# Performance work log

Hardware: AMD Instinct MI355X
Metric: run time of the kernel (lower is better)

Reference implementation:

```python
import jax, jax.numpy as jnp
import numpy as np

EPS = 1e-4  # SPDRectifiedLinear eigenvalue threshold
POOL = 17   # adaptive pool output size


def setup_inputs() -> dict:
    key = jax.random.key(0)
    ks = jax.random.split(key, 6)
    B, Cin, H, W = 32, 2048, 34, 34
    Cr = 256
    feat_dim = Cr * (Cr + 1) // 2  # 32896
    x = jax.random.normal(ks[0], (B, Cin, H, W), dtype=jnp.float32)
    W_red = jax.random.normal(ks[1], (Cr, Cin), dtype=jnp.float32) * (1.0 / np.sqrt(Cin))
    W1 = jax.random.normal(ks[2], (256, feat_dim), dtype=jnp.float32) * (1.0 / np.sqrt(feat_dim))
    b1 = jax.random.normal(ks[3], (256,), dtype=jnp.float32) * 0.01
    W2 = jax.random.normal(ks[4], (3, 256), dtype=jnp.float32) * (1.0 / np.sqrt(256.0))
    b2 = jax.random.normal(ks[5], (3,), dtype=jnp.float32) * 0.01
    return {"x": x, "W_red": W_red, "W1": W1, "b1": b1, "W2": W2, "b2": b2}


def reference(x, W_red, W1, b1, W2, b2):
    B, Cin, H, W = x.shape
    # AdaptiveAvgPool2d((17,17)) with H=W=34 is exactly a uniform 2x2 avg pool
    f = x.reshape(B, Cin, POOL, H // POOL, POOL, W // POOL).mean(axis=(3, 5))  # [B,Cin,17,17]
    # 1x1 conv (no bias) == channel-mixing matmul
    f = jnp.einsum('bchw,dc->bdhw', f, W_red)  # [B,Cr,17,17]
    Cr = f.shape[1]
    f = f.reshape(B, Cr, -1).transpose(0, 2, 1)  # [B, N=289, Cr]
    N = f.shape[1]
    # batch covariance over spatial positions (unbiased)
    xc = f - f.mean(axis=1, keepdims=True)
    cov = jnp.einsum('bnc,bnd->bcd', xc, xc) / (N - 1)  # [B,Cr,Cr] SPD
    # SPD ReLU (eigenvalue clamp at EPS) followed by SPD logmap (matrix log)
    # share one eigendecomposition: same eigenvectors for both ops
    w, v = jnp.linalg.eigh(cov)
    w = jnp.log(jnp.clip(w, EPS))
    cov = jnp.einsum('bic,bc,bjc->bij', v, w, v)  # log-mapped symmetric matrix
    # SPD flatten: upper triangle, off-diagonal scaled by sqrt(2)
    iu, ju = jnp.triu_indices(Cr)
    scale = jnp.where(iu == ju, 1.0, jnp.sqrt(2.0)).astype(cov.dtype)
    flat = cov[:, iu, ju] * scale  # [B, Cr*(Cr+1)/2]
    # classifier MLP
    h = jax.nn.relu(flat @ W1.T + b1)
    return h @ W2.T + b2  # [B, num_classes]
```

## Files before the change

### kernel.cpp

```cpp
#include <hip/hip_runtime.h>
#include <math.h>


#define SWEEPS 7
#define NROUNDS (SWEEPS * 15)

#define P_OFF     0
#define A_OFF     0
#define V_OFF     8388608
#define U_OFF     16777216
#define LOGW_OFF  17825792
#define MEAN_OFF  79691776
#define F_OFF     83558400
#define FLAT_OFF  83558400
#define PART_OFF  93519872
#define H_OFF     94568448
#define WS_REQUIRED 94601216

__device__ __forceinline__ void pair16(int r, int t, int& p, int& q) {
    if (t == 0) { p = 0; q = 1 + r; return; }
    int u = r + t; if (u >= 15) u -= 15;
    int v = r - t; if (v < 0) v += 15;
    p = 1 + u; q = 1 + v;
    if (p > q) { int w = p; p = q; q = w; }
}
__device__ __forceinline__ void pair32(int rr, int t, int& p, int& q) {
    if (t == 0) { p = 0; q = 1 + rr; return; }
    int u = rr + t; if (u >= 31) u -= 31;
    int v = rr - t; if (v < 0) v += 31;
    p = 1 + u; q = 1 + v;
    if (p > q) { int w = p; p = q; q = w; }
}

__global__ __launch_bounds__(256) void k_pool(const float* __restrict__ x, float* __restrict__ P) {
    int c = blockIdx.x, b = blockIdx.y;
    const float* xs = x + (size_t)(b * 2048 + c) * 1156;
    float* ps = P + (size_t)(b * 2048 + c) * 304;
    for (int n = threadIdx.x; n < 289; n += 256) {
        int i = n / 17, j = n % 17;
        int base = (2 * i) * 34 + 2 * j;
        ps[n] = 0.25f * (xs[base] + xs[base + 1] + xs[base + 34] + xs[base + 35]);
    }
}

__global__ __launch_bounds__(256) void k_gemm_red(const float* __restrict__ P,
                                                  const float* __restrict__ Wr,
                                                  float* __restrict__ f) {
    __shared__ float Wt[32][33];
    __shared__ float Pt[32][64];
    int nt = blockIdx.x, dt = blockIdx.y, b = blockIdx.z;
    int n0 = nt * 64, d0 = dt * 32;
    int tid = threadIdx.x;
    int ty = tid >> 4, tx = tid & 15;
    float acc[2][4] = {};
    for (int c0 = 0; c0 < 2048; c0 += 32) {
        __syncthreads();
        for (int idx = tid; idx < 32 * 32; idx += 256) {
            int r = idx >> 5, cc = idx & 31;
            Wt[r][cc] = Wr[(size_t)(d0 + r) * 2048 + c0 + cc];
        }
        for (int idx = tid; idx < 32 * 64; idx += 256) {
            int r = idx >> 6, cc = idx & 63;
            int n = n0 + cc;
            Pt[r][cc] = (n < 289) ? P[(size_t)(b * 2048 + c0 + r) * 304 + n] : 0.0f;
        }
        __syncthreads();
#pragma unroll
        for (int kk = 0; kk < 32; ++kk) {
            float a0 = Wt[ty * 2 + 0][kk], a1 = Wt[ty * 2 + 1][kk];
            float p0 = Pt[kk][tx * 4 + 0], p1 = Pt[kk][tx * 4 + 1];
            float p2 = Pt[kk][tx * 4 + 2], p3 = Pt[kk][tx * 4 + 3];
            acc[0][0] += a0 * p0; acc[0][1] += a0 * p1; acc[0][2] += a0 * p2; acc[0][3] += a0 * p3;
            acc[1][0] += a1 * p0; acc[1][1] += a1 * p1; acc[1][2] += a1 * p2; acc[1][3] += a1 * p3;
        }
    }
    for (int ii = 0; ii < 2; ++ii)
        for (int jj = 0; jj < 4; ++jj) {
            int d = d0 + ty * 2 + ii, n = n0 + tx * 4 + jj;
            if (n < 289) f[(size_t)(b * 256 + d) * 304 + n] = acc[ii][jj];
        }
}

__global__ __launch_bounds__(256) void k_mean(const float* __restrict__ f, float* __restrict__ mean) {
    int row = blockIdx.x * 4 + (threadIdx.x >> 6);
    int lane = threadIdx.x & 63;
    const float* fr = f + (size_t)row * 304;
    double s = 0.0;
    for (int n = lane; n < 289; n += 64) s += (double)fr[n];
    for (int off = 32; off; off >>= 1) s += __shfl_down(s, off);
    if (lane == 0) mean[row] = (float)(s / 289.0);
}

__global__ __launch_bounds__(256) void k_cov(const float* __restrict__ f,
                                             const float* __restrict__ mean,
                                             float* __restrict__ A) {
    __shared__ float Fi[32][33];
    __shared__ float Fj[32][33];
    int b = blockIdx.x, tp = blockIdx.y;
    int ti = (int)((sqrtf(8.0f * tp + 1.0f) - 1.0f) * 0.5f);
    while (ti * (ti + 1) / 2 > tp) --ti;
    while ((ti + 1) * (ti + 2) / 2 <= tp) ++ti;
    int tj = tp - ti * (ti + 1) / 2;
    int tid = threadIdx.x;
    int tyy = tid >> 4, txx = tid & 15;
    bool diag = (ti == tj);
    double acc[2][2] = {};
    for (int nc = 0; nc < 289; nc += 32) {
        __syncthreads();
        for (int idx = tid; idx < 32 * 32; idx += 256) {
            int r = idx >> 5, k = idx & 31;
            int n = nc + k;
            int d1 = ti * 32 + r;
            Fi[r][k] = (n < 289) ? f[(size_t)(b * 256 + d1) * 304 + n] - mean[b * 256 + d1] : 0.0f;
            if (!diag) {
                int d2 = tj * 32 + r;
                Fj[r][k] = (n < 289) ? f[(size_t)(b * 256 + d2) * 304 + n] - mean[b * 256 + d2] : 0.0f;
            }
        }
        __syncthreads();
        const float(*FJ)[33] = diag ? Fi : Fj;
#pragma unroll 8
        for (int kk = 0; kk < 32; ++kk) {
            float a0 = Fi[tyy * 2 + 0][kk], a1 = Fi[tyy * 2 + 1][kk];
            float c0 = FJ[txx * 2 + 0][kk], c1 = FJ[txx * 2 + 1][kk];
            acc[0][0] += (double)a0 * c0; acc[0][1] += (double)a0 * c1;
            acc[1][0] += (double)a1 * c0; acc[1][1] += (double)a1 * c1;
        }
    }
    for (int ii = 0; ii < 2; ++ii)
        for (int jj = 0; jj < 2; ++jj) {
            int i = ti * 32 + tyy * 2 + ii, j = tj * 32 + txx * 2 + jj;
            float v = (float)(acc[ii][jj] * (1.0 / 288.0));
            A[((size_t)b << 16) + i * 256 + j] = v;
            if (!diag) A[((size_t)b << 16) + j * 256 + i] = v;
        }
}

__global__ __launch_bounds__(256) void k_init_v(float* __restrict__ V) {
    int i = blockIdx.x, b = blockIdx.y, j = threadIdx.x;
    V[((size_t)b << 16) + i * 256 + j] = (i == j) ? 1.0f : 0.0f;
}

__global__ __launch_bounds__(256) void k_inner(const float* __restrict__ A,
                                               float* __restrict__ Ubuf, int r) {
    __shared__ float S[32][33], UU[32][33];
    __shared__ float cbuf[16], sbuf[16];
    __shared__ int pbuf[16], qbuf[16];
    __shared__ float rednorm[8];
    int g = blockIdx.x, b = blockIdx.y;
    int tid = threadIdx.x;
    int bp, bq; pair16(r, g, bp, bq);
    const float* Ab = A + ((size_t)b << 16);
    for (int e = tid; e < 1024; e += 256) {
        int i = e >> 5, j = e & 31;
        int ri = (i < 16) ? bp * 16 + i : bq * 16 + i - 16;
        int rj = (j < 16) ? bp * 16 + j : bq * 16 + j - 16;
        S[i][j] = Ab[ri * 256 + rj];
        UU[i][j] = (i == j) ? 1.0f : 0.0f;
    }
    __syncthreads();
    for (int sw = 0; sw < 6; ++sw) {
        float off = 0.0f, dia = 0.0f;
        for (int e = tid; e < 1024; e += 256) {
            int i = e >> 5, j = e & 31; float v = S[i][j];
            if (i == j) dia += v * v; else off += v * v;
        }
        for (int o = 32; o; o >>= 1) { off += __shfl_down(off, o); dia += __shfl_down(dia, o); }
        if ((tid & 63) == 0) { rednorm[tid >> 6] = off; rednorm[4 + (tid >> 6)] = dia; }
        __syncthreads();
        off = rednorm[0] + rednorm[1] + rednorm[2] + rednorm[3];
        dia = rednorm[4] + rednorm[5] + rednorm[6] + rednorm[7];
        __syncthreads();
        if (off <= 1e-13f * fmaxf(dia, 1e-30f)) break;
        for (int rr = 0; rr < 31; ++rr) {
            if (tid < 16) {
                int p, q; pair32(rr, tid, p, q);
                float app = S[p][p], aqq = S[q][q], apq = S[p][q];
                float c = 1.0f, s = 0.0f;
                if (apq * apq > 1e-36f) {
                    float tau = (aqq - app) / (2.0f * apq);
                    float t = 1.0f / (fabsf(tau) + sqrtf(1.0f + tau * tau));
                    if (tau < 0.0f) t = -t;
                    c = rsqrtf(1.0f + t * t); s = t * c;
                }
                cbuf[tid] = c; sbuf[tid] = s; pbuf[tid] = p; qbuf[tid] = q;
            }
            __syncthreads();
            {
                int i = tid & 31, t0 = (tid >> 5) * 2;
#pragma unroll
                for (int m = 0; m < 2; ++m) {
                    int t = t0 + m;
                    int p = pbuf[t], q = qbuf[t];
                    float c = cbuf[t], s = sbuf[t];
                    float x = S[i][p], y = S[i][q];
                    S[i][p] = c * x - s * y; S[i][q] = s * x + c * y;
                    x = UU[i][p]; y = UU[i][q];
                    UU[i][p] = c * x - s * y; UU[i][q] = s * x + c * y;
                }
            }
            __syncthreads();
            {
                int j = tid & 31, t0 = (tid >> 5) * 2;
#pragma unroll
                for (int m = 0; m < 2; ++m) {
                    int t = t0 + m;
                    int p = pbuf[t], q = qbuf[t];
                    float c = cbuf[t], s = sbuf[t];
                    float x = S[p][j], y = S[q][j];
                    S[p][j] = c * x - s * y; S[q][j] = s * x + c * y;
                }
            }
            __syncthreads();
        }
    }
    for (int e = tid; e < 1024; e += 256)
        Ubuf[(((size_t)b * 8 + g) << 10) + e] = UU[e >> 5][e & 31];
}

__global__ __launch_bounds__(64) void k_update(float* __restrict__ A, float* __restrict__ V,
                                               const float* __restrict__ Ubuf, int r) {
    __shared__ float U1[32][33], U2[32][33], TT[32][33];
    int task = blockIdx.x, b = blockIdx.y;
    int l = threadIdx.x;
    int lr = l >> 3, lc = l & 7;
    int a0 = lr * 4, c0 = lc * 4;
    if (task < 64) {
        int gk = task >> 3, gl = task & 7;
        int pk, qk, pl, ql;
        pair16(r, gk, pk, qk); pair16(r, gl, pl, ql);
        const float* Uk = Ubuf + (((size_t)b * 8 + gk) << 10);
        const float* Ul = Ubuf + (((size_t)b * 8 + gl) << 10);
        float* Ab = A + ((size_t)b << 16);
        for (int e = l; e < 1024; e += 64) {
            int i = e >> 5, j = e & 31;
            U1[i][j] = Uk[e];
            U2[i][j] = Ul[e];
            int ri = (i < 16) ? pk * 16 + i : qk * 16 + i - 16;
            int rj = (j < 16) ? pl * 16 + j : ql * 16 + j - 16;
            TT[i][j] = Ab[ri * 256 + rj];
        }
        __syncthreads();
        float acc[4][4] = {};
#pragma unroll 4
        for (int k = 0; k < 32; ++k) {
            float u0 = U1[k][a0], u1 = U1[k][a0 + 1], u2 = U1[k][a0 + 2], u3 = U1[k][a0 + 3];
            float t0 = TT[k][c0], t1 = TT[k][c0 + 1], t2 = TT[k][c0 + 2], t3 = TT[k][c0 + 3];
            acc[0][0] += u0 * t0; acc[0][1] += u0 * t1; acc[0][2] += u0 * t2; acc[0][3] += u0 * t3;
            acc[1][0] += u1 * t0; acc[1][1] += u1 * t1; acc[1][2] += u1 * t2; acc[1][3] += u1 * t3;
            acc[2][0] += u2 * t0; acc[2][1] += u2 * t1; acc[2][2] += u2 * t2; acc[2][3] += u2 * t3;
            acc[3][0] += u3 * t0; acc[3][1] += u3 * t1; acc[3][2] += u3 * t2; acc[3][3] += u3 * t3;
        }
        __syncthreads();
#pragma unroll
        for (int i = 0; i < 4; ++i)
#pragma unroll
            for (int j = 0; j < 4; ++j) TT[a0 + i][c0 + j] = acc[i][j];
        __syncthreads();
        float acc2[4][4] = {};
#pragma unroll 4
        for (int k = 0; k < 32; ++k) {
            float w0 = TT[a0][k], w1 = TT[a0 + 1][k], w2 = TT[a0 + 2][k], w3 = TT[a0 + 3][k];
            float u0 = U2[k][c0], u1 = U2[k][c0 + 1], u2 = U2[k][c0 + 2], u3 = U2[k][c0 + 3];
            acc2[0][0] += w0 * u0; acc2[0][1] += w0 * u1; acc2[0][2] += w0 * u2; acc2[0][3] += w0 * u3;
            acc2[1][0] += w1 * u0; acc2[1][1] += w1 * u1; acc2[1][2] += w1 * u2; acc2[1][3] += w1 * u3;
            acc2[2][0] += w2 * u0; acc2[2][1] += w2 * u1; acc2[2][2] += w2 * u2; acc2[2][3] += w2 * u3;
            acc2[3][0] += w3 * u0; acc2[3][1] += w3 * u1; acc2[3][2] += w3 * u2; acc2[3][3] += w3 * u3;
        }
#pragma unroll
        for (int i = 0; i < 4; ++i) {
            int ga = a0 + i; int ri = (ga < 16) ? pk * 16 + ga : qk * 16 + ga - 16;
#pragma unroll
            for (int j = 0; j < 4; ++j) {
                int gc = c0 + j; int rj = (gc < 16) ? pl * 16 + gc : ql * 16 + gc - 16;
                Ab[ri * 256 + rj] = acc2[i][j];
            }
        }
    } else {
        int t2 = task - 64;
        int rb = t2 >> 3, gl = t2 & 7;
        int pl, ql; pair16(r, gl, pl, ql);
        const float* Ul = Ubuf + (((size_t)b * 8 + gl) << 10);
        float* Vb = V + ((size_t)b << 16);
        for (int e = l; e < 1024; e += 64) {
            int i = e >> 5, j = e & 31;
            U2[i][j] = Ul[e];
            int rj = (j < 16) ? pl * 16 + j : ql * 16 + j - 16;
            TT[i][j] = Vb[(rb * 32 + i) * 256 + rj];
        }
        __syncthreads();
        float acc2[4][4] = {};
#pragma unroll 4
        for (int k = 0; k < 32; ++k) {
            float w0 = TT[a0][k], w1 = TT[a0 + 1][k], w2 = TT[a0 + 2][k], w3 = TT[a0 + 3][k];
            float u0 = U2[k][c0], u1 = U2[k][c0 + 1], u2 = U2[k][c0 + 2], u3 = U2[k][c0 + 3];
            acc2[0][0] += w0 * u0; acc2[0][1] += w0 * u1; acc2[0][2] += w0 * u2; acc2[0][3] += w0 * u3;
            acc2[1][0] += w1 * u0; acc2[1][1] += w1 * u1; acc2[1][2] += w1 * u2; acc2[1][3] += w1 * u3;
            acc2[2][0] += w2 * u0; acc2[2][1] += w2 * u1; acc2[2][2] += w2 * u2; acc2[2][3] += w2 * u3;
            acc2[3][0] += w3 * u0; acc2[3][1] += w3 * u1; acc2[3][2] += w3 * u2; acc2[3][3] += w3 * u3;
        }
#pragma unroll
        for (int i = 0; i < 4; ++i)
#pragma unroll
            for (int j = 0; j < 4; ++j) {
                int gc = c0 + j; int rj = (gc < 16) ? pl * 16 + gc : ql * 16 + gc - 16;
                Vb[(rb * 32 + a0 + i) * 256 + rj] = acc2[i][j];
            }
    }
}

__global__ __launch_bounds__(256) void k_logw(const float* __restrict__ A, float* __restrict__ logw) {
    int b = blockIdx.x, k = threadIdx.x;
    logw[b * 256 + k] = logf(fmaxf(A[((size_t)b << 16) + k * 257], 1e-4f));
}

__global__ __launch_bounds__(256) void k_vlogv(const float* __restrict__ V,
                                               const float* __restrict__ logw,
                                               float* __restrict__ flat) {
    __shared__ float Vi[32][33], Vjw[32][33];
    int t = blockIdx.x, b = blockIdx.y;
    int ti = 0;
    while (t >= 8 - ti) { t -= 8 - ti; ++ti; }
    int tj = ti + t;
    int tid = threadIdx.x;
    int ty = tid >> 4, tx = tid & 15;
    const float* Vb = V + ((size_t)b << 16);
    const float* wb = logw + b * 256;
    float acc[2][2] = {};
    for (int kc = 0; kc < 8; ++kc) {
        __syncthreads();
        for (int e = tid; e < 1024; e += 256) {
            int rr = e >> 5, cc = e & 31;
            Vi[rr][cc] = Vb[(ti * 32 + rr) * 256 + kc * 32 + cc];
            Vjw[rr][cc] = Vb[(tj * 32 + rr) * 256 + kc * 32 + cc] * wb[kc * 32 + cc];
        }
        __syncthreads();
#pragma unroll 8
        for (int k = 0; k < 32; ++k) {
            float a0 = Vi[ty * 2][k], a1 = Vi[ty * 2 + 1][k];
            float b0 = Vjw[tx * 2][k], b1 = Vjw[tx * 2 + 1][k];
            acc[0][0] += a0 * b0; acc[0][1] += a0 * b1;
            acc[1][0] += a1 * b0; acc[1][1] += a1 * b1;
        }
    }
    const float SQ2 = 1.41421356237309515f;
    float* flatb = flat + (size_t)b * 32896;
#pragma unroll
    for (int ii = 0; ii < 2; ++ii)
#pragma unroll
        for (int jj = 0; jj < 2; ++jj) {
            int gi = ti * 32 + ty * 2 + ii, gj = tj * 32 + tx * 2 + jj;
            if (gi <= gj) {
                int fidx = gi * 256 - gi * (gi - 1) / 2 + (gj - gi);
                flatb[fidx] = acc[ii][jj] * ((gi == gj) ? 1.0f : SQ2);
            }
        }
}

__global__ __launch_bounds__(256) void k_mlp1(const float* __restrict__ flat,
                                              const float* __restrict__ W1,
                                              float* __restrict__ partial) {
    __shared__ float Fl[32][65];
    __shared__ float Wl[32][65];
    int ec = blockIdx.x, jt = blockIdx.y;
    int tid = threadIdx.x;
    int e0 = ec * 1028;
    float acc[4] = {};
    for (int ch = 0; ch < 1028; ch += 64) {
        __syncthreads();
        for (int idx = tid; idx < 2048; idx += 256) {
            int row = idx >> 6, col = idx & 63;
            int e = ch + col;
            float fv = 0.0f, wv = 0.0f;
            if (e < 1028) {
                fv = flat[(size_t)row * 32896 + e0 + e];
                wv = W1[(size_t)(jt * 32 + row) * 32896 + e0 + e];
            }
            Fl[row][col] = fv; Wl[row][col] = wv;
        }
        __syncthreads();
#pragma unroll 4
        for (int ee = 0; ee < 64; ++ee) {
#pragma unroll
            for (int pp = 0; pp < 4; ++pp) {
                int pair = tid + pp * 256;
                acc[pp] += Wl[pair >> 5][ee] * Fl[pair & 31][ee];
            }
        }
    }
    for (int pp = 0; pp < 4; ++pp)
        partial[((size_t)(jt * 32 + ec) << 10) + tid + pp * 256] = acc[pp];
}

__global__ __launch_bounds__(1024) void k_mlp1red(const float* __restrict__ partial,
                                                  const float* __restrict__ b1,
                                                  float* __restrict__ h) {
    int jt = blockIdx.x, tid = threadIdx.x;
    float acc = 0.0f;
    for (int ec = 0; ec < 32; ++ec) acc += partial[((size_t)(jt * 32 + ec) << 10) + tid];
    int j = jt * 32 + (tid >> 5), bI = tid & 31;
    h[bI * 256 + j] = fmaxf(acc + b1[j], 0.0f);
}

__global__ __launch_bounds__(128) void k_mlp2(const float* __restrict__ h,
                                              const float* __restrict__ W2,
                                              const float* __restrict__ b2,
                                              float* __restrict__ out) {
    int tid = threadIdx.x;
    if (tid >= 96) return;
    int bI = tid / 3, cls = tid % 3;
    double acc = (double)b2[cls];
    for (int j = 0; j < 256; ++j) acc += (double)h[bI * 256 + j] * (double)W2[cls * 256 + j];
    out[tid] = (float)acc;
}

extern "C" void kernel_launch(void* const* d_in, const int* in_sizes, int n_in,
                              void* d_out, int out_size, void* d_ws, size_t ws_size,
                              hipStream_t stream) {
    const float* x  = (const float*)d_in[0];
    const float* Wr = (const float*)d_in[1];
    const float* W1 = (const float*)d_in[2];
    const float* b1 = (const float*)d_in[3];
    const float* W2 = (const float*)d_in[4];
    const float* b2 = (const float*)d_in[5];
    float* out = (float*)d_out;
    char* ws = (char*)d_ws;
    if (ws_size < (size_t)WS_REQUIRED) return;

    float* P    = (float*)(ws + P_OFF);
    float* A    = (float*)(ws + A_OFF);
    float* V    = (float*)(ws + V_OFF);
    float* Ubuf = (float*)(ws + U_OFF);
    float* logw = (float*)(ws + LOGW_OFF);
    float* mean = (float*)(ws + MEAN_OFF);
    float* f    = (float*)(ws + F_OFF);
    float* flat = (float*)(ws + FLAT_OFF);
    float* part = (float*)(ws + PART_OFF);
    float* h    = (float*)(ws + H_OFF);

    k_pool<<<dim3(2048, 32), 256, 0, stream>>>(x, P);
    k_gemm_red<<<dim3(5, 8, 32), 256, 0, stream>>>(P, Wr, f);
    k_mean<<<2048, 256, 0, stream>>>(f, mean);
    k_cov<<<dim3(32, 36), 256, 0, stream>>>(f, mean, A);
    k_init_v<<<dim3(256, 32), 256, 0, stream>>>(V);
    for (int r = 0; r < NROUNDS; ++r) {
        int rr = r % 15;
        k_inner<<<dim3(8, 32), 256, 0, stream>>>(A, Ubuf, rr);
        k_update<<<dim3(128, 32), 64, 0, stream>>>(A, V, Ubuf, rr);
    }
    k_logw<<<32, 256, 0, stream>>>(A, logw);
    k_vlogv<<<dim3(36, 32), 256, 0, stream>>>(V, logw, flat);
    k_mlp1<<<dim3(32, 8), 256, 0, stream>>>(flat, W1, part);
    k_mlp1red<<<8, 1024, 0, stream>>>(part, b1, h);
    k_mlp2<<<1, 128, 0, stream>>>(h, W2, b2, out);
}
```

Before: 12.68 ms.

## Fuse Jacobi rounds into one persistent cooperative kernel with grid sync

Replaces the 210 alternating k_inner/k_update launches, plus the V-init and logw kernels, with a single cooperative kernel of 256 blocks that loops over all rounds and separates phases with grid.sync(). Each block handles one inner 32x32 subproblem and then four update tasks, using four 64-thread sub-groups with separate shared tiles. This removes per-launch overhead and the gaps between kernels. In exchange, grid-wide barriers have their own cost, the update phase now runs on only 256 blocks instead of 4096, and shared memory per block grows considerably.

New measurement: 17.44 ms. 1.38x slower.

```diff
diff --git a/kernel.cpp b/kernel.cpp
--- a/kernel.cpp
+++ b/kernel.cpp
@@ -1,5 +1,8 @@
 #include <hip/hip_runtime.h>
+#include <hip/hip_cooperative_groups.h>
 #include <math.h>
+
+namespace cg = cooperative_groups;
 
 
 #define SWEEPS 7
@@ -136,182 +139,202 @@
         }
 }
 
-__global__ __launch_bounds__(256) void k_init_v(float* __restrict__ V) {
-    int i = blockIdx.x, b = blockIdx.y, j = threadIdx.x;
-    V[((size_t)b << 16) + i * 256 + j] = (i == j) ? 1.0f : 0.0f;
-}
-
-__global__ __launch_bounds__(256) void k_inner(const float* __restrict__ A,
-                                               float* __restrict__ Ubuf, int r) {
+__global__ __launch_bounds__(256) void k_jacobi(float* __restrict__ A,
+                                                float* __restrict__ V,
+                                                float* __restrict__ Ubuf,
+                                                float* __restrict__ logw) {
+    cg::grid_group grid = cg::this_grid();
     __shared__ float S[32][33], UU[32][33];
     __shared__ float cbuf[16], sbuf[16];
     __shared__ int pbuf[16], qbuf[16];
     __shared__ float rednorm[8];
-    int g = blockIdx.x, b = blockIdx.y;
-    int tid = threadIdx.x;
-    int bp, bq; pair16(r, g, bp, bq);
-    const float* Ab = A + ((size_t)b << 16);
-    for (int e = tid; e < 1024; e += 256) {
-        int i = e >> 5, j = e & 31;
-        int ri = (i < 16) ? bp * 16 + i : bq * 16 + i - 16;
-        int rj = (j < 16) ? bp * 16 + j : bq * 16 + j - 16;
-        S[i][j] = Ab[ri * 256 + rj];
-        UU[i][j] = (i == j) ? 1.0f : 0.0f;
-    }
-    __syncthreads();
-    for (int sw = 0; sw < 6; ++sw) {
-        float off = 0.0f, dia = 0.0f;
-        for (int e = tid; e < 1024; e += 256) {
-            int i = e >> 5, j = e & 31; float v = S[i][j];
-            if (i == j) dia += v * v; else off += v * v;
-        }
-        for (int o = 32; o; o >>= 1) { off += __shfl_down(off, o); dia += __shfl_down(dia, o); }
-        if ((tid & 63) == 0) { rednorm[tid >> 6] = off; rednorm[4 + (tid >> 6)] = dia; }
-        __syncthreads();
-        off = rednorm[0] + rednorm[1] + rednorm[2] + rednorm[3];
-        dia = rednorm[4] + rednorm[5] + rednorm[6] + rednorm[7];
-        __syncthreads();
-        if (off <= 1e-13f * fmaxf(dia, 1e-30f)) break;
-        for (int rr = 0; rr < 31; ++rr) {
-            if (tid < 16) {
-                int p, q; pair32(rr, tid, p, q);
-                float app = S[p][p], aqq = S[q][q], apq = S[p][q];
-                float c = 1.0f, s = 0.0f;
-                if (apq * apq > 1e-36f) {
-                    float tau = (aqq - app) / (2.0f * apq);
-                    float t = 1.0f / (fabsf(tau) + sqrtf(1.0f + tau * tau));
-                    if (tau < 0.0f) t = -t;
-                    c = rsqrtf(1.0f + t * t); s = t * c;
+    __shared__ float U1[4][32][33], U2[4][32][33], TT[4][32][33];
+
+    const int blk = blockIdx.x;
+    const int b = blk >> 3, g = blk & 7;
+    const int tid = threadIdx.x;
+
+    {
+        float* Vb = V + ((size_t)b << 16) + (size_t)(g * 32) * 256;
+        for (int e = tid; e < 8192; e += 256) {
+            int i = e >> 8, j = e & 255;
+            Vb[i * 256 + j] = ((g * 32 + i) == j) ? 1.0f : 0.0f;
+        }
+    }
+
+    for (int r = 0; r < NROUNDS; ++r) {
+        const int rr = r % 15;
+
+        {
+            int bp, bq; pair16(rr, g, bp, bq);
+            const float* Ab = A + ((size_t)b << 16);
+            for (int e = tid; e < 1024; e += 256) {
+                int i = e >> 5, j = e & 31;
+                int ri = (i < 16) ? bp * 16 + i : bq * 16 + i - 16;
+                int rj = (j < 16) ? bp * 16 + j : bq * 16 + j - 16;
+                S[i][j] = Ab[ri * 256 + rj];
+                UU[i][j] = (i == j) ? 1.0f : 0.0f;
+            }
+            __syncthreads();
+            for (int sw = 0; sw < 6; ++sw) {
+                float off = 0.0f, dia = 0.0f;
+                for (int e = tid; e < 1024; e += 256) {
+                    int i = e >> 5, j = e & 31; float v = S[i][j];
+                    if (i == j) dia += v * v; else off += v * v;
                 }
-                cbuf[tid] = c; sbuf[tid] = s; pbuf[tid] = p; qbuf[tid] = q;
-            }
-            __syncthreads();
-            {
-                int i = tid & 31, t0 = (tid >> 5) * 2;
-#pragma unroll
-                for (int m = 0; m < 2; ++m) {
-                    int t = t0 + m;
-                    int p = pbuf[t], q = qbuf[t];
-                    float c = cbuf[t], s = sbuf[t];
-                    float x = S[i][p], y = S[i][q];
-                    S[i][p] = c * x - s * y; S[i][q] = s * x + c * y;
-                    x = UU[i][p]; y = UU[i][q];
-                    UU[i][p] = c * x - s * y; UU[i][q] = s * x + c * y;
+                for (int o = 32; o; o >>= 1) { off += __shfl_down(off, o); dia += __shfl_down(dia, o); }
+                if ((tid & 63) == 0) { rednorm[tid >> 6] = off; rednorm[4 + (tid >> 6)] = dia; }
+                __syncthreads();
+                off = rednorm[0] + rednorm[1] + rednorm[2] + rednorm[3];
+                dia = rednorm[4] + rednorm[5] + rednorm[6] + rednorm[7];
+                __syncthreads();
+                if (off <= 1e-13f * fmaxf(dia, 1e-30f)) break;
+                for (int rot = 0; rot < 31; ++rot) {
+                    if (tid < 16) {
+                        int p, q; pair32(rot, tid, p, q);
+                        float app = S[p][p], aqq = S[q][q], apq = S[p][q];
+                        float c = 1.0f, s = 0.0f;
+                        if (apq * apq > 1e-36f) {
+                            float tau = (aqq - app) / (2.0f * apq);
+                            float t = 1.0f / (fabsf(tau) + sqrtf(1.0f + tau * tau));
+                            if (tau < 0.0f) t = -t;
+                            c = rsqrtf(1.0f + t * t); s = t * c;
+                        }
+                        cbuf[tid] = c; sbuf[tid] = s; pbuf[tid] = p; qbuf[tid] = q;
+                    }
+                    __syncthreads();
+                    {
+                        int i = tid & 31, t0 = (tid >> 5) * 2;
+#pragma unroll
+                        for (int m = 0; m < 2; ++m) {
+                            int t = t0 + m;
+                            int p = pbuf[t], q = qbuf[t];
+                            float c = cbuf[t], s = sbuf[t];
+                            float x = S[i][p], y = S[i][q];
+                            S[i][p] = c * x - s * y; S[i][q] = s * x + c * y;
+                            x = UU[i][p]; y = UU[i][q];
+                            UU[i][p] = c * x - s * y; UU[i][q] = s * x + c * y;
+                        }
+                    }
+                    __syncthreads();
+                    {
+                        int j = tid & 31, t0 = (tid >> 5) * 2;
+#pragma unroll
+                        for (int m = 0; m < 2; ++m) {
+                            int t = t0 + m;
+                            int p = pbuf[t], q = qbuf[t];
+                            float c = cbuf[t], s = sbuf[t];
+                            float x = S[p][j], y = S[q][j];
+                            S[p][j] = c * x - s * y; S[q][j] = s * x + c * y;
+                        }
+                    }
+                    __syncthreads();
                 }
             }
-            __syncthreads();
-            {
-                int j = tid & 31, t0 = (tid >> 5) * 2;
-#pragma unroll
-                for (int m = 0; m < 2; ++m) {
-                    int t = t0 + m;
-                    int p = pbuf[t], q = qbuf[t];
-                    float c = cbuf[t], s = sbuf[t];
-                    float x = S[p][j], y = S[q][j];
-                    S[p][j] = c * x - s * y; S[q][j] = s * x + c * y;
+            for (int e = tid; e < 1024; e += 256)
+                Ubuf[(((size_t)b * 8 + g) << 10) + e] = UU[e >> 5][e & 31];
+        }
+        grid.sync();
+
+        {
+            const int sub = tid >> 6, l = tid & 63;
+            const int lr = l >> 3, lc = l & 7;
+            const int a0 = lr * 4, c0 = lc * 4;
+            float (*u1)[33] = U1[sub];
+            float (*u2)[33] = U2[sub];
+            float (*tt)[33] = TT[sub];
+            for (int pass = 0; pass < 4; ++pass) {
+                const int T = (blk << 4) + (pass << 2) + sub;
+                const int b2 = T >> 7, task = T & 127;
+                if (task < 64) {
+                    int gk = task >> 3, gl = task & 7;
+                    int pk, qk, pl, ql;
+                    pair16(rr, gk, pk, qk); pair16(rr, gl, pl, ql);
+                    const float* Uk = Ubuf + (((size_t)b2 * 8 + gk) << 10);
+                    const float* Ul = Ubuf + (((size_t)b2 * 8 + gl) << 10);
+                    float* Ab = A + ((size_t)b2 << 16);
+                    for (int e = l; e < 1024; e += 64) {
+                        int i = e >> 5, j = e & 31;
+                        u1[i][j] = Uk[e];
+                        u2[i][j] = Ul[e];
+                        int ri = (i < 16) ? pk * 16 + i : qk * 16 + i - 16;
+                        int rj = (j < 16) ? pl * 16 + j : ql * 16 + j - 16;
+                        tt[i][j] = Ab[ri * 256 + rj];
+                    }
+                    __syncthreads();
+                    float acc[4][4] = {};
+#pragma unroll 4
+                    for (int k = 0; k < 32; ++k) {
+                        float w0 = u1[k][a0], w1 = u1[k][a0 + 1], w2 = u1[k][a0 + 2], w3 = u1[k][a0 + 3];
+                        float t0 = tt[k][c0], t1 = tt[k][c0 + 1], t2 = tt[k][c0 + 2], t3 = tt[k][c0 + 3];
+                        acc[0][0] += w0 * t0; acc[0][1] += w0 * t1; acc[0][2] += w0 * t2; acc[0][3] += w0 * t3;
+                        acc[1][0] += w1 * t0; acc[1][1] += w1 * t1; acc[1][2] += w1 * t2; acc[1][3] += w1 * t3;
+                        acc[2][0] += w2 * t0; acc[2][1] += w2 * t1; acc[2][2] += w2 * t2; acc[2][3] += w2 * t3;
+                        acc[3][0] += w3 * t0; acc[3][1] += w3 * t1; acc[3][2] += w3 * t2; acc[3][3] += w3 * t3;
+                    }
+                    __syncthreads();
+#pragma unroll
+                    for (int i = 0; i < 4; ++i)
+#pragma unroll
+                        for (int j = 0; j < 4; ++j) tt[a0 + i][c0 + j] = acc[i][j];
+                    __syncthreads();
+                    float acc2[4][4] = {};
+#pragma unroll 4
+                    for (int k = 0; k < 32; ++k) {
+                        float w0 = tt[a0][k], w1 = tt[a0 + 1][k], w2 = tt[a0 + 2][k], w3 = tt[a0 + 3][k];
+                        float u0 = u2[k][c0], u1v = u2[k][c0 + 1], u2v = u2[k][c0 + 2], u3 = u2[k][c0 + 3];
+                        acc2[0][0] += w0 * u0; acc2[0][1] += w0 * u1v; acc2[0][2] += w0 * u2v; acc2[0][3] += w0 * u3;
+                        acc2[1][0] += w1 * u0; acc2[1][1] += w1 * u1v; acc2[1][2] += w1 * u2v; acc2[1][3] += w1 * u3;
+                        acc2[2][0] += w2 * u0; acc2[2][1] += w2 * u1v; acc2[2][2] += w2 * u2v; acc2[2][3] += w2 * u3;
+                        acc2[3][0] += w3 * u0; acc2[3][1] += w3 * u1v; acc2[3][2] += w3 * u2v; acc2[3][3] += w3 * u3;
+                    }
+#pragma unroll
+                    for (int i = 0; i < 4; ++i) {
+                        int ga = a0 + i; int ri = (ga < 16) ? pk * 16 + ga : qk * 16 + ga - 16;
+#pragma unroll
+                        for (int j = 0; j < 4; ++j) {
+                            int gc = c0 + j; int rj = (gc < 16) ? pl * 16 + gc : ql * 16 + gc - 16;
+                            Ab[ri * 256 + rj] = acc2[i][j];
+                        }
+                    }
+                } else {
+                    int t2 = task - 64;
+                    int rb = t2 >> 3, gl = t2 & 7;
+                    int pl, ql; pair16(rr, gl, pl, ql);
+                    const float* Ul = Ubuf + (((size_t)b2 * 8 + gl) << 10);
+                    float* Vb = V + ((size_t)b2 << 16);
+                    for (int e = l; e < 1024; e += 64) {
+                        int i = e >> 5, j = e & 31;
+                        u2[i][j] = Ul[e];
+                        int rj = (j < 16) ? pl * 16 + j : ql * 16 + j - 16;
+                        tt[i][j] = Vb[(rb * 32 + i) * 256 + rj];
+                    }
+                    __syncthreads();
+                    float acc2[4][4] = {};
+#pragma unroll 4
+                    for (int k = 0; k < 32; ++k) {
+                        float w0 = tt[a0][k], w1 = tt[a0 + 1][k], w2 = tt[a0 + 2][k], w3 = tt[a0 + 3][k];
+                        float u0 = u2[k][c0], u1v = u2[k][c0 + 1], u2v = u2[k][c0 + 2], u3 = u2[k][c0 + 3];
+                        acc2[0][0] += w0 * u0; acc2[0][1] += w0 * u1v; acc2[0][2] += w0 * u2v; acc2[0][3] += w0 * u3;
+                        acc2[1][0] += w1 * u0; acc2[1][1] += w1 * u1v; acc2[1][2] += w1 * u2v; acc2[1][3] += w1 * u3;
+                        acc2[2][0] += w2 * u0; acc2[2][1] += w2 * u1v; acc2[2][2] += w2 * u2v; acc2[2][3] += w2 * u3;
+                        acc2[3][0] += w3 * u0; acc2[3][1] += w3 * u1v; acc2[3][2] += w3 * u2v; acc2[3][3] += w3 * u3;
+                    }
+#pragma unroll
+                    for (int i = 0; i < 4; ++i)
+#pragma unroll
+                        for (int j = 0; j < 4; ++j) {
+                            int gc = c0 + j; int rj = (gc < 16) ? pl * 16 + gc : ql * 16 + gc - 16;
+                            Vb[(rb * 32 + a0 + i) * 256 + rj] = acc2[i][j];
+                        }
                 }
             }
-            __syncthreads();
-        }
-    }
-    for (int e = tid; e < 1024; e += 256)
-        Ubuf[(((size_t)b * 8 + g) << 10) + e] = UU[e >> 5][e & 31];
-}
-
-__global__ __launch_bounds__(64) void k_update(float* __restrict__ A, float* __restrict__ V,
-                                               const float* __restrict__ Ubuf, int r) {
-    __shared__ float U1[32][33], U2[32][33], TT[32][33];
-    int task = blockIdx.x, b = blockIdx.y;
-    int l = threadIdx.x;
-    int lr = l >> 3, lc = l & 7;
-    int a0 = lr * 4, c0 = lc * 4;
-    if (task < 64) {
-        int gk = task >> 3, gl = task & 7;
-        int pk, qk, pl, ql;
-        pair16(r, gk, pk, qk); pair16(r, gl, pl, ql);
-        const float* Uk = Ubuf + (((size_t)b * 8 + gk) << 10);
-        const float* Ul = Ubuf + (((size_t)b * 8 + gl) << 10);
-        float* Ab = A + ((size_t)b << 16);
-        for (int e = l; e < 1024; e += 64) {
-            int i = e >> 5, j = e & 31;
-            U1[i][j] = Uk[e];
-            U2[i][j] = Ul[e];
-            int ri = (i < 16) ? pk * 16 + i : qk * 16 + i - 16;
-            int rj = (j < 16) ? pl * 16 + j : ql * 16 + j - 16;
-            TT[i][j] = Ab[ri * 256 + rj];
-        }
-        __syncthreads();
-        float acc[4][4] = {};
-#pragma unroll 4
-        for (int k = 0; k < 32; ++k) {
-            float u0 = U1[k][a0], u1 = U1[k][a0 + 1], u2 = U1[k][a0 + 2], u3 = U1[k][a0 + 3];
-            float t0 = TT[k][c0], t1 = TT[k][c0 + 1], t2 = TT[k][c0 + 2], t3 = TT[k][c0 + 3];
-            acc[0][0] += u0 * t0; acc[0][1] += u0 * t1; acc[0][2] += u0 * t2; acc[0][3] += u0 * t3;
-            acc[1][0] += u1 * t0; acc[1][1] += u1 * t1; acc[1][2] += u1 * t2; acc[1][3] += u1 * t3;
-            acc[2][0] += u2 * t0; acc[2][1] += u2 * t1; acc[2][2] += u2 * t2; acc[2][3] += u2 * t3;
-            acc[3][0] += u3 * t0; acc[3][1] += u3 * t1; acc[3][2] += u3 * t2; acc[3][3] += u3 * t3;
-        }
-        __syncthreads();
-#pragma unroll
-        for (int i = 0; i < 4; ++i)
-#pragma unroll
-            for (int j = 0; j < 4; ++j) TT[a0 + i][c0 + j] = acc[i][j];
-        __syncthreads();
-        float acc2[4][4] = {};
-#pragma unroll 4
-        for (int k = 0; k < 32; ++k) {
-            float w0 = TT[a0][k], w1 = TT[a0 + 1][k], w2 = TT[a0 + 2][k], w3 = TT[a0 + 3][k];
-            float u0 = U2[k][c0], u1 = U2[k][c0 + 1], u2 = U2[k][c0 + 2], u3 = U2[k][c0 + 3];
-            acc2[0][0] += w0 * u0; acc2[0][1] += w0 * u1; acc2[0][2] += w0 * u2; acc2[0][3] += w0 * u3;
-            acc2[1][0] += w1 * u0; acc2[1][1] += w1 * u1; acc2[1][2] += w1 * u2; acc2[1][3] += w1 * u3;
-            acc2[2][0] += w2 * u0; acc2[2][1] += w2 * u1; acc2[2][2] += w2 * u2; acc2[2][3] += w2 * u3;
-            acc2[3][0] += w3 * u0; acc2[3][1] += w3 * u1; acc2[3][2] += w3 * u2; acc2[3][3] += w3 * u3;
-        }
-#pragma unroll
-        for (int i = 0; i < 4; ++i) {
-            int ga = a0 + i; int ri = (ga < 16) ? pk * 16 + ga : qk * 16 + ga - 16;
-#pragma unroll
-            for (int j = 0; j < 4; ++j) {
-                int gc = c0 + j; int rj = (gc < 16) ? pl * 16 + gc : ql * 16 + gc - 16;
-                Ab[ri * 256 + rj] = acc2[i][j];
-            }
-        }
-    } else {
-        int t2 = task - 64;
-        int rb = t2 >> 3, gl = t2 & 7;
-        int pl, ql; pair16(r, gl, pl, ql);
-        const float* Ul = Ubuf + (((size_t)b * 8 + gl) << 10);
-        float* Vb = V + ((size_t)b << 16);
-        for (int e = l; e < 1024; e += 64) {
-            int i = e >> 5, j = e & 31;
-            U2[i][j] = Ul[e];
-            int rj = (j < 16) ? pl * 16 + j : ql * 16 + j - 16;
-            TT[i][j] = Vb[(rb * 32 + i) * 256 + rj];
-        }
-        __syncthreads();
-        float acc2[4][4] = {};
-#pragma unroll 4
-        for (int k = 0; k < 32; ++k) {
-            float w0 = TT[a0][k], w1 = TT[a0 + 1][k], w2 = TT[a0 + 2][k], w3 = TT[a0 + 3][k];
-            float u0 = U2[k][c0], u1 = U2[k][c0 + 1], u2 = U2[k][c0 + 2], u3 = U2[k][c0 + 3];
-            acc2[0][0] += w0 * u0; acc2[0][1] += w0 * u1; acc2[0][2] += w0 * u2; acc2[0][3] += w0 * u3;
-            acc2[1][0] += w1 * u0; acc2[1][1] += w1 * u1; acc2[1][2] += w1 * u2; acc2[1][3] += w1 * u3;
-            acc2[2][0] += w2 * u0; acc2[2][1] += w2 * u1; acc2[2][2] += w2 * u2; acc2[2][3] += w2 * u3;
-            acc2[3][0] += w3 * u0; acc2[3][1] += w3 * u1; acc2[3][2] += w3 * u2; acc2[3][3] += w3 * u3;
-        }
-#pragma unroll
-        for (int i = 0; i < 4; ++i)
-#pragma unroll
-            for (int j = 0; j < 4; ++j) {
-                int gc = c0 + j; int rj = (gc < 16) ? pl * 16 + gc : ql * 16 + gc - 16;
-                Vb[(rb * 32 + a0 + i) * 256 + rj] = acc2[i][j];
-            }
-    }
-}
-
-__global__ __launch_bounds__(256) void k_logw(const float* __restrict__ A, float* __restrict__ logw) {
-    int b = blockIdx.x, k = threadIdx.x;
-    logw[b * 256 + k] = logf(fmaxf(A[((size_t)b << 16) + k * 257], 1e-4f));
+        }
+        grid.sync();
+    }
+
+    if (g == 0)
+        logw[b * 256 + tid] = logf(fmaxf(A[((size_t)b << 16) + tid * 257], 1e-4f));
 }
 
 __global__ __launch_bounds__(256) void k_vlogv(const float* __restrict__ V,
@@ -442,13 +465,11 @@
     k_gemm_red<<<dim3(5, 8, 32), 256, 0, stream>>>(P, Wr, f);
     k_mean<<<2048, 256, 0, stream>>>(f, mean);
     k_cov<<<dim3(32, 36), 256, 0, stream>>>(f, mean, A);
-    k_init_v<<<dim3(256, 32), 256, 0, stream>>>(V);
-    for (int r = 0; r < NROUNDS; ++r) {
-        int rr = r % 15;
-        k_inner<<<dim3(8, 32), 256, 0, stream>>>(A, Ubuf, rr);
-        k_update<<<dim3(128, 32), 64, 0, stream>>>(A, V, Ubuf, rr);
-    }
-    k_logw<<<32, 256, 0, stream>>>(A, logw);
+    {
+        void* args[] = { (void*)&A, (void*)&V, (void*)&Ubuf, (void*)&logw };
+        hipLaunchCooperativeKernel((const void*)k_jacobi, dim3(256), dim3(256),
+                                   args, 0, stream);
+    }
     k_vlogv<<<dim3(36, 32), 256, 0, stream>>>(V, logw, flat);
     k_mlp1<<<dim3(32, 8), 256, 0, stream>>>(flat, W1, part);
     k_mlp1red<<<8, 1024, 0, stream>>>(part, b1, h);
```
